# Kernel optimization log

Hardware: AMD Instinct MI355X
Metric: run time of the kernel (lower is better)

## Reference

```python
import jax, jax.numpy as jnp
import numpy as np
import math

N_NODES = 64000
N_GRAPHS = 512
HIDDEN = 128
CLUSTERS = 10
NUM_FILTER = 16
N_CLASSES = 2
S_HID = math.ceil((HIDDEN + CLUSTERS) / 2)  # 69
P_HID = 8


def _mlp2(x, w1, b1, w2, b2):
    # 2-layer MLP: Linear -> ReLU -> Linear (matches MLP(2, in, hid, out))
    return jax.nn.relu(x @ w1 + b1) @ w2 + b2


def setup_inputs() -> dict:
    key = jax.random.key(0)
    ks = jax.random.split(key, 12)
    # node embeddings (output of get_emb)
    H_all = jax.random.normal(ks[0], (N_NODES, HIDDEN), dtype=jnp.float32)
    # graph indicator: 125 nodes per graph, sorted (as produced by batching)
    batch = jnp.repeat(jnp.arange(N_GRAPHS, dtype=jnp.int32), N_NODES // N_GRAPHS)
    targets = jax.random.randint(ks[1], (N_GRAPHS,), 0, N_CLASSES, dtype=jnp.int32)
    s = 0.05
    # S_mlp: hidden -> S_HID -> clusters
    w1 = jax.random.normal(ks[2], (HIDDEN, S_HID), dtype=jnp.float32) * s
    b1 = jnp.zeros((S_HID,), dtype=jnp.float32)
    w2 = jax.random.normal(ks[3], (S_HID, CLUSTERS), dtype=jnp.float32) * s
    b2 = jnp.zeros((CLUSTERS,), dtype=jnp.float32)
    # final: hidden*clusters -> 2
    wf = jax.random.normal(ks[4], (HIDDEN * CLUSTERS, N_CLASSES), dtype=jnp.float32) * s
    bf = jnp.zeros((N_CLASSES,), dtype=jnp.float32)
    # prototype_features_MLP: hidden -> 8 -> num_graph_filter
    p1 = jax.random.normal(ks[5], (HIDDEN, P_HID), dtype=jnp.float32) * s
    pb1 = jnp.zeros((P_HID,), dtype=jnp.float32)
    p2 = jax.random.normal(ks[6], (P_HID, NUM_FILTER), dtype=jnp.float32) * s
    pb2 = jnp.zeros((NUM_FILTER,), dtype=jnp.float32)
    # correlation parameters (initialized like the torch module)
    corr_inter = jax.nn.softmax(jax.random.uniform(ks[7], (N_CLASSES, NUM_FILTER)), axis=0)
    corr_intra = jax.nn.softmax(jax.random.uniform(ks[8], (N_CLASSES, NUM_FILTER)), axis=1)
    return {"H_all": H_all, "batch": batch, "targets": targets,
            "w1": w1, "b1": b1, "w2": w2, "b2": b2,
            "wf": wf, "bf": bf,
            "p1": p1, "pb1": pb1, "p2": p2, "pb2": pb2,
            "corr_inter": corr_inter, "corr_intra": corr_intra}


def reference(H_all, batch, targets, w1, b1, w2, b2, wf, bf,
              p1, pb1, p2, pb2, corr_inter, corr_intra):
    # per-node soft cluster assignment  [N, C]
    S_all = jax.nn.softmax(_mlp2(H_all, w1, b1, w2, b2), axis=-1)
    # segment matmul E_g = S_g^T @ H_g  -> [B, C, D] via segment-reduced outer products
    outer = S_all[:, :, None] * H_all[:, None, :]  # [N, C, D]
    E_all = jax.ops.segment_sum(outer, batch, num_segments=N_GRAPHS)
    B = E_all.shape[0]
    pred1 = E_all.reshape(B, -1) @ wf + bf  # dropout off (eval)
    p = jax.nn.softmax(pred1, axis=-1)
    # multinomial sample from pred_softmax (no grad)
    key = jax.random.key(42)
    sample = jax.random.categorical(key, jnp.log(jax.lax.stop_gradient(p) + 1e-12), axis=-1)
    ind_positive_sample = sample == targets
    oh = jax.nn.one_hot(sample, N_CLASSES, dtype=p.dtype)
    epsilon = jax.lax.stop_gradient(jnp.where(oh != 0, 1.0 - p, -p))
    sample_cat_oh = p + epsilon  # straight-through one-hot
    Q = jax.nn.softmax(_mlp2(E_all, p1, pb1, p2, pb2), axis=-1)  # [B, C, F]
    correlation = jax.nn.softmax(corr_inter, axis=0) * jax.nn.softmax(corr_intra, axis=1)  # [2, F]
    correlation_mask = sample_cat_oh @ correlation  # [B, F]
    feature_mask = jnp.sum(Q * correlation_mask[:, None, :], axis=-1)  # [B, C]
    E_masked = feature_mask[:, :, None] * E_all  # einsum('bi,bij->bij')
    pred2 = E_masked.reshape(B, -1) @ wf + bf
    return (pred1, pred2, ind_positive_sample, S_all, E_all, Q)
```

## Files before the change

kernel.cpp:

```cpp
#include <hip/hip_runtime.h>

#define NN 64000
#define NG 512
#define NPG 125
#define DIM 128
#define NC 10
#define SHID 69
#define NF 16
#define PHID 8
#define ELPAD 132
#define TSTR 85
#define PSTR 41
#define EPSTR 11

#define OFF_PRED1 0
#define OFF_PRED2 1024
#define OFF_IND   2048
#define OFF_S     2560
#define OFF_E     642560
#define OFF_Q     1297920

typedef __attribute__((ext_vector_type(8))) short short8;
typedef __attribute__((ext_vector_type(4))) float f32x4;

__device__ __forceinline__ unsigned rotl32(unsigned x, int r) {
    return (x << r) | (x >> (32 - r));
}

__device__ __forceinline__ void threefry_0_42(unsigned x0, unsigned x1,
                                              unsigned& o0, unsigned& o1) {
    const unsigned k0 = 0u, k1 = 42u;
    const unsigned k2 = k0 ^ k1 ^ 0x1BD11BDAu;
    unsigned ks[3] = {k0, k1, k2};
    const int R0[4] = {13, 15, 26, 6};
    const int R1[4] = {17, 29, 16, 24};
    x0 += k0; x1 += k1;
    #pragma unroll
    for (int i = 0; i < 5; i++) {
        const int* R = (i & 1) ? R1 : R0;
        #pragma unroll
        for (int r = 0; r < 4; r++) {
            x0 += x1;
            x1 = rotl32(x1, R[r]);
            x1 ^= x0;
        }
        x0 += ks[(i + 1) % 3];
        x1 += ks[(i + 2) % 3] + (unsigned)(i + 1);
    }
    o0 = x0; o1 = x1;
}

__device__ __forceinline__ unsigned random_bits_partitionable(unsigned i) {
    unsigned o0, o1;
    threefry_0_42(0u, i, o0, o1);
    return o0 ^ o1;
}

__device__ __forceinline__ float gumbel_from_bits(unsigned bits) {
    float f = __uint_as_float((bits >> 9) | 0x3f800000u) - 1.0f;
    if (f <= 0.0f) f = 1.1754943508222875e-38f;
    return -logf(-logf(f));
}

#define R10(M) M(0) M(1) M(2) M(3) M(4) M(5) M(6) M(7) M(8) M(9)

__global__ __launch_bounds__(256) void k_split_w1(
    const float* __restrict__ w1, short* __restrict__ fragHi,
    short* __restrict__ fragLo) {
    int e = blockIdx.x * 256 + threadIdx.x;
    int s = e >> 3, i = e & 7;
    int jt = s >> 8, ks = (s >> 6) & 3, l = s & 63;
    int j = jt * 16 + (l & 15);
    int kb = ks * 32 + ((l >> 4) & 3) * 8;
    float x = (j < SHID) ? w1[(kb + i) * SHID + j] : 0.0f;
    unsigned u = __float_as_uint(x);
    short hi = (short)(u >> 16);
    float hf = __uint_as_float(u & 0xFFFF0000u);
    short lo = (short)(__float_as_uint(x - hf) >> 16);
    fragHi[s * 8 + i] = hi;
    fragLo[s * 8 + i] = lo;
}

__global__ __launch_bounds__(256, 4) void k_node_mlp(
    const float* __restrict__ H, const short* __restrict__ fragHi,
    const short* __restrict__ fragLo,
    const float* __restrict__ b1, const float* __restrict__ w2,
    const float* __restrict__ b2, float* __restrict__ S) {
    __shared__ __align__(16) float Ts[64 * TSTR];
    __shared__ float Ps[64 * PSTR];
    int tid = threadIdx.x;
    int w = tid >> 6, l = tid & 63;
    int node = blockIdx.x * 64 + w * 16 + (l & 15);
    const float* Hp = H + (size_t)node * DIM + ((l >> 4) & 3) * 8;

    short8 aHi[4], aLo[4];
    #pragma unroll
    for (int ks = 0; ks < 4; ks++) {
        float4 x0 = *(const float4*)(Hp + ks * 32);
        float4 x1 = *(const float4*)(Hp + ks * 32 + 4);
        float xs[8] = {x0.x, x0.y, x0.z, x0.w, x1.x, x1.y, x1.z, x1.w};
        #pragma unroll
        for (int i = 0; i < 8; i++) {
            unsigned u = __float_as_uint(xs[i]);
            aHi[ks][i] = (short)(u >> 16);
            float lo = xs[i] - __uint_as_float(u & 0xFFFF0000u);
            aLo[ks][i] = (short)(__float_as_uint(lo) >> 16);
        }
    }

    f32x4 acc[5];
    #pragma unroll
    for (int jt = 0; jt < 5; jt++) {
        f32x4 a = {0.f, 0.f, 0.f, 0.f};
        #pragma unroll
        for (int ks = 0; ks < 4; ks++) {
            int slot = (jt * 4 + ks) * 64 + l;
            short8 bh = *(const short8*)(fragHi + (size_t)slot * 8);
            short8 bl = *(const short8*)(fragLo + (size_t)slot * 8);
            a = __builtin_amdgcn_mfma_f32_16x16x32_bf16(aHi[ks], bh, a, 0, 0, 0);
            a = __builtin_amdgcn_mfma_f32_16x16x32_bf16(aLo[ks], bh, a, 0, 0, 0);
            a = __builtin_amdgcn_mfma_f32_16x16x32_bf16(aHi[ks], bl, a, 0, 0, 0);
        }
        acc[jt] = a;
    }

    #pragma unroll
    for (int jt = 0; jt < 5; jt++) {
        int j = jt * 16 + (l & 15);
        float bj = (j < SHID) ? b1[j] : 0.0f;
        #pragma unroll
        for (int r = 0; r < 4; r++) {
            int m = w * 16 + ((l >> 4) & 3) * 4 + r;
            float tv = acc[jt][r];
            Ts[m * TSTR + j] = (j < SHID) ? fmaxf(tv + bj, 0.0f) : 0.0f;
        }
    }
    __syncthreads();

    {
        int n = tid & 63, q = tid >> 6;
        float lg[NC] = {};
        for (int jj = 0; jj < 18; jj++) {
            int j = q * 18 + jj;
            int jx = (j < SHID) ? j : (SHID - 1);
            float tr = Ts[n * TSTR + j];
            const float* w2r = w2 + jx * NC;
            #pragma unroll
            for (int c = 0; c < NC; c++) lg[c] = fmaf(tr, w2r[c], lg[c]);
        }
        #pragma unroll
        for (int c = 0; c < NC; c++) Ps[n * PSTR + q * NC + c] = lg[c];
    }
    __syncthreads();

    if (tid < 64) {
        int n = tid;
        const float* pr = &Ps[n * PSTR];
        #define LD(c) float s##c = pr[c] + pr[10 + c] + pr[20 + c] + pr[30 + c] + b2[c];
        R10(LD)
        #undef LD
        float m = fmaxf(fmaxf(fmaxf(s0, s1), fmaxf(s2, s3)),
                        fmaxf(fmaxf(fmaxf(s4, s5), fmaxf(s6, s7)), fmaxf(s8, s9)));
        float e0 = expf(s0 - m), e1 = expf(s1 - m), e2 = expf(s2 - m),
              e3 = expf(s3 - m), e4 = expf(s4 - m), e5 = expf(s5 - m),
              e6 = expf(s6 - m), e7 = expf(s7 - m), e8 = expf(s8 - m),
              e9 = expf(s9 - m);
        float ssum = ((e0 + e1) + (e2 + e3)) + ((e4 + e5) + (e6 + e7)) + (e8 + e9);
        float inv = 1.0f / ssum;
        float2* Sp2 = (float2*)(S + ((size_t)blockIdx.x * 64 + n) * NC);
        Sp2[0] = make_float2(e0 * inv, e1 * inv);
        Sp2[1] = make_float2(e2 * inv, e3 * inv);
        Sp2[2] = make_float2(e4 * inv, e5 * inv);
        Sp2[3] = make_float2(e6 * inv, e7 * inv);
        Sp2[4] = make_float2(e8 * inv, e9 * inv);
    }
}

__global__ __launch_bounds__(1024, 4) void k_E_tail(
    const float* __restrict__ H, const float* __restrict__ S,
    const float* __restrict__ wf, const float* __restrict__ bf,
    const int* __restrict__ targets,
    const float* __restrict__ p1, const float* __restrict__ pb1,
    const float* __restrict__ p2, const float* __restrict__ pb2,
    const float* __restrict__ ci, const float* __restrict__ cr,
    float* __restrict__ E, float* __restrict__ pred1, float* __restrict__ pred2,
    float* __restrict__ ind, float* __restrict__ Q) {
    __shared__ __align__(8) float Sl[128 * NC];
    __shared__ float Epart[7 * 128 * EPSTR];
    __shared__ __align__(16) float El[NC * ELPAD];
    __shared__ float fmbuf[NC];
    int g = blockIdx.x, tid = threadIdx.x;

    const float* Sg = S + (size_t)g * NPG * NC;
    for (int i = tid; i < 128 * NC; i += 1024) Sl[i] = (i < NPG * NC) ? Sg[i] : 0.0f;
    __syncthreads();

    int q = tid >> 7;
    int d = tid & 127;
    const float* Hg = H + (size_t)g * NPG * DIM + d;

    #define DECLA(c) float a##c = 0.f;
    R10(DECLA)
    #undef DECLA
    int n0 = q * 16;
    #pragma unroll
    for (int ib = 0; ib < 16; ib += 8) {
        float h[8];
        #pragma unroll
        for (int u = 0; u < 8; u++) {
            int nh = min(n0 + ib + u, NPG - 1);
            h[u] = Hg[(size_t)nh * DIM];
        }
        #pragma unroll
        for (int u = 0; u < 8; u++) {
            const float2* S2 = (const float2*)(Sl + (n0 + ib + u) * NC);
            float2 s01 = S2[0], s23 = S2[1], s45 = S2[2], s67 = S2[3], s89 = S2[4];
            a0 = fmaf(s01.x, h[u], a0); a1 = fmaf(s01.y, h[u], a1);
            a2 = fmaf(s23.x, h[u], a2); a3 = fmaf(s23.y, h[u], a3);
            a4 = fmaf(s45.x, h[u], a4); a5 = fmaf(s45.y, h[u], a5);
            a6 = fmaf(s67.x, h[u], a6); a7 = fmaf(s67.y, h[u], a7);
            a8 = fmaf(s89.x, h[u], a8); a9 = fmaf(s89.y, h[u], a9);
        }
    }
    if (q > 0) {
        float* ep = &Epart[((q - 1) * 128 + d) * EPSTR];
        #define STP(c) ep[c] = a##c;
        R10(STP)
        #undef STP
    }
    __syncthreads();
    if (q == 0) {
        float* Eo = E + (size_t)g * (NC * DIM) + d;
        #pragma unroll
        for (int k = 0; k < 7; k++) {
            const float* ep = &Epart[(k * 128 + d) * EPSTR];
            a0 += ep[0]; a1 += ep[1]; a2 += ep[2]; a3 += ep[3]; a4 += ep[4];
            a5 += ep[5]; a6 += ep[6]; a7 += ep[7]; a8 += ep[8]; a9 += ep[9];
        }
        #define CMB(c) { El[(c) * ELPAD + d] = a##c; Eo[(c) * DIM] = a##c; }
        R10(CMB)
        #undef CMB
    }
    __syncthreads();

    const float2* wf2 = (const float2*)wf;
    int l = tid;
    int samp = 0;
    float corr_lf = 0.f;

    if (tid < 64) {
        if (l < 32) {
            int i = l >> 4, f = l & 15;
            float a = ci[f], b = ci[NF + f];
            float mm = fmaxf(a, b);
            float ea = expf(a - mm), eb = expf(b - mm);
            float inter = expf(ci[i * NF + f] - mm) / (ea + eb);
            float mi = -1e30f;
            for (int j = 0; j < NF; j++) mi = fmaxf(mi, cr[i * NF + j]);
            float ri = 0.f;
            for (int j = 0; j < NF; j++) ri += expf(cr[i * NF + j] - mi);
            float intra = expf(cr[i * NF + f] - mi) / ri;
            corr_lf = inter * intra;
        }

        float a0 = 0.f, a1 = 0.f;
        #pragma unroll
        for (int i = 0; i < 20; i++) {
            int idx = i * 64 + l;
            float e = El[(idx >> 7) * ELPAD + (idx & 127)];
            float2 w = wf2[idx];
            a0 = fmaf(e, w.x, a0);
            a1 = fmaf(e, w.y, a1);
        }
        #pragma unroll
        for (int off = 32; off > 0; off >>= 1) {
            a0 += __shfl_down(a0, off);
            a1 += __shfl_down(a1, off);
        }
        if (l == 0) {
            float y0 = a0 + bf[0], y1 = a1 + bf[1];
            pred1[g * 2] = y0;
            pred1[g * 2 + 1] = y1;
            float m = fmaxf(y0, y1);
            float e0 = expf(y0 - m), e1 = expf(y1 - m), s = e0 + e1;
            float p0 = e0 / s, pp1 = e1 / s;
            float g0 = gumbel_from_bits(random_bits_partitionable(2 * g));
            float g1 = gumbel_from_bits(random_bits_partitionable(2 * g + 1));
            float l0 = logf(p0 + 1e-12f) + g0;
            float l1 = logf(pp1 + 1e-12f) + g1;
            samp = (l1 > l0) ? 1 : 0;
            ind[g] = (samp == targets[g]) ? 1.0f : 0.0f;
        }
        samp = __shfl(samp, 0);

        if (l < 40) {
            int p = l >> 2, s = l & 3;
            float ua = pb1[2 * s], ub = pb1[2 * s + 1];
            const float4* E4 = (const float4*)&El[p * ELPAD];
            #pragma unroll 4
            for (int k4 = 0; k4 < 32; k4++) {
                float4 e4 = E4[k4];
                float es[4] = {e4.x, e4.y, e4.z, e4.w};
                #pragma unroll
                for (int kk = 0; kk < 4; kk++) {
                    int k = k4 * 4 + kk;
                    ua = fmaf(es[kk], p1[k * PHID + 2 * s], ua);
                    ub = fmaf(es[kk], p1[k * PHID + 2 * s + 1], ub);
                }
            }
            ua = fmaxf(ua, 0.f);
            ub = fmaxf(ub, 0.f);
            float v[NF];
            #pragma unroll
            for (int f = 0; f < NF; f++) {
                v[f] = pb2[f] * 0.25f;
                v[f] = fmaf(ua, p2[(2 * s) * NF + f], v[f]);
                v[f] = fmaf(ub, p2[(2 * s + 1) * NF + f], v[f]);
            }
            #pragma unroll
            for (int f = 0; f < NF; f++) {
                v[f] += __shfl_xor(v[f], 1);
                v[f] += __shfl_xor(v[f], 2);
            }
            float m = v[0];
            #pragma unroll
            for (int f = 1; f < NF; f++) m = fmaxf(m, v[f]);
            float ssum = 0.f, qv[NF];
            #pragma unroll
            for (int f = 0; f < NF; f++) { qv[f] = expf(v[f] - m); ssum += qv[f]; }
            float inv = 1.0f / ssum;
            #pragma unroll
            for (int f = 0; f < NF; f++) qv[f] *= inv;
            float* Qo = Q + ((size_t)g * NC + p) * NF;
            ((float4*)Qo)[s] = make_float4(qv[s * 4], qv[s * 4 + 1], qv[s * 4 + 2], qv[s * 4 + 3]);
            float fmv = 0.f;
            #pragma unroll
            for (int f = 0; f < NF; f++) {
                float cv = __shfl(corr_lf, samp * NF + f);
                fmv = fmaf(qv[f], cv, fmv);
            }
            if (s == 0) fmbuf[p] = fmv;
        }
    }
    __syncthreads();

    if (tid < 64) {
        float b0 = 0.f, b1acc = 0.f;
        #pragma unroll
        for (int i = 0; i < 20; i++) {
            int idx = i * 64 + l;
            float e = El[(idx >> 7) * ELPAD + (idx & 127)] * fmbuf[idx >> 7];
            float2 w = wf2[idx];
            b0 = fmaf(e, w.x, b0);
            b1acc = fmaf(e, w.y, b1acc);
        }
        #pragma unroll
        for (int off = 32; off > 0; off >>= 1) {
            b0 += __shfl_down(b0, off);
            b1acc += __shfl_down(b1acc, off);
        }
        if (l == 0) {
            pred2[g * 2] = b0 + bf[0];
            pred2[g * 2 + 1] = b1acc + bf[1];
        }
    }
}

extern "C" void kernel_launch(void* const* d_in, const int* in_sizes, int n_in,
                              void* d_out, int out_size, void* d_ws, size_t ws_size,
                              hipStream_t stream) {
    const float* H       = (const float*)d_in[0];
    const int*   targets = (const int*)d_in[2];
    const float* w1      = (const float*)d_in[3];
    const float* b1      = (const float*)d_in[4];
    const float* w2      = (const float*)d_in[5];
    const float* b2      = (const float*)d_in[6];
    const float* wf      = (const float*)d_in[7];
    const float* bf      = (const float*)d_in[8];
    const float* p1      = (const float*)d_in[9];
    const float* pb1     = (const float*)d_in[10];
    const float* p2      = (const float*)d_in[11];
    const float* pb2     = (const float*)d_in[12];
    const float* ci      = (const float*)d_in[13];
    const float* cr      = (const float*)d_in[14];

    float* out   = (float*)d_out;
    float* pred1 = out + OFF_PRED1;
    float* pred2 = out + OFF_PRED2;
    float* ind   = out + OFF_IND;
    float* S     = out + OFF_S;
    float* E     = out + OFF_E;
    float* Q     = out + OFF_Q;

    short* fragHi = (short*)d_ws;
    short* fragLo = (short*)((char*)d_ws + 20480);

    k_split_w1<<<40, 256, 0, stream>>>(w1, fragHi, fragLo);
    k_node_mlp<<<NN / 64, 256, 0, stream>>>(H, fragHi, fragLo, b1, w2, b2, S);
    k_E_tail<<<NG, 1024, 0, stream>>>(H, S, wf, bf, targets, p1, pb1, p2, pb2,
                                      ci, cr, E, pred1, pred2, ind, Q);
}
```

Measured before the change: 132.6 us.

## Fuse node MLP softmax into per-graph segment-sum kernel

Merges the per-node MLP/softmax kernel with the per-graph E/tail kernel, so each 512-thread block computes S for its graph's 125 nodes, keeps it in shared memory, then reduces the outer products. This removes a kernel launch and the global round trip of S, and H rows are read twice within the same block, likely hitting cache. The second layer of the MLP now runs in registers with cross-lane shuffles instead of shared-memory staging. Only 512 blocks of 512 threads are launched, which lowers parallelism for the MFMA phase and gives each thread more serial work.

```diff
diff --git a/kernel.cpp b/kernel.cpp
--- a/kernel.cpp
+++ b/kernel.cpp
@@ -9,8 +9,6 @@
 #define NF 16
 #define PHID 8
 #define ELPAD 132
-#define TSTR 85
-#define PSTR 41
 #define EPSTR 11
 
 #define OFF_PRED1 0
@@ -81,176 +79,188 @@
     fragLo[s * 8 + i] = lo;
 }
 
-__global__ __launch_bounds__(256, 4) void k_node_mlp(
+__global__ __launch_bounds__(512, 2) void k_fused(
     const float* __restrict__ H, const short* __restrict__ fragHi,
     const short* __restrict__ fragLo,
     const float* __restrict__ b1, const float* __restrict__ w2,
-    const float* __restrict__ b2, float* __restrict__ S) {
-    __shared__ __align__(16) float Ts[64 * TSTR];
-    __shared__ float Ps[64 * PSTR];
-    int tid = threadIdx.x;
-    int w = tid >> 6, l = tid & 63;
-    int node = blockIdx.x * 64 + w * 16 + (l & 15);
-    const float* Hp = H + (size_t)node * DIM + ((l >> 4) & 3) * 8;
-
-    short8 aHi[4], aLo[4];
-    #pragma unroll
-    for (int ks = 0; ks < 4; ks++) {
-        float4 x0 = *(const float4*)(Hp + ks * 32);
-        float4 x1 = *(const float4*)(Hp + ks * 32 + 4);
-        float xs[8] = {x0.x, x0.y, x0.z, x0.w, x1.x, x1.y, x1.z, x1.w};
-        #pragma unroll
-        for (int i = 0; i < 8; i++) {
-            unsigned u = __float_as_uint(xs[i]);
-            aHi[ks][i] = (short)(u >> 16);
-            float lo = xs[i] - __uint_as_float(u & 0xFFFF0000u);
-            aLo[ks][i] = (short)(__float_as_uint(lo) >> 16);
-        }
-    }
-
-    f32x4 acc[5];
-    #pragma unroll
-    for (int jt = 0; jt < 5; jt++) {
-        f32x4 a = {0.f, 0.f, 0.f, 0.f};
-        #pragma unroll
-        for (int ks = 0; ks < 4; ks++) {
-            int slot = (jt * 4 + ks) * 64 + l;
-            short8 bh = *(const short8*)(fragHi + (size_t)slot * 8);
-            short8 bl = *(const short8*)(fragLo + (size_t)slot * 8);
-            a = __builtin_amdgcn_mfma_f32_16x16x32_bf16(aHi[ks], bh, a, 0, 0, 0);
-            a = __builtin_amdgcn_mfma_f32_16x16x32_bf16(aLo[ks], bh, a, 0, 0, 0);
-            a = __builtin_amdgcn_mfma_f32_16x16x32_bf16(aHi[ks], bl, a, 0, 0, 0);
-        }
-        acc[jt] = a;
-    }
-
-    #pragma unroll
-    for (int jt = 0; jt < 5; jt++) {
-        int j = jt * 16 + (l & 15);
-        float bj = (j < SHID) ? b1[j] : 0.0f;
-        #pragma unroll
-        for (int r = 0; r < 4; r++) {
-            int m = w * 16 + ((l >> 4) & 3) * 4 + r;
-            float tv = acc[jt][r];
-            Ts[m * TSTR + j] = (j < SHID) ? fmaxf(tv + bj, 0.0f) : 0.0f;
-        }
-    }
-    __syncthreads();
-
-    {
-        int n = tid & 63, q = tid >> 6;
-        float lg[NC] = {};
-        for (int jj = 0; jj < 18; jj++) {
-            int j = q * 18 + jj;
-            int jx = (j < SHID) ? j : (SHID - 1);
-            float tr = Ts[n * TSTR + j];
-            const float* w2r = w2 + jx * NC;
-            #pragma unroll
-            for (int c = 0; c < NC; c++) lg[c] = fmaf(tr, w2r[c], lg[c]);
-        }
-        #pragma unroll
-        for (int c = 0; c < NC; c++) Ps[n * PSTR + q * NC + c] = lg[c];
-    }
-    __syncthreads();
-
-    if (tid < 64) {
-        int n = tid;
-        const float* pr = &Ps[n * PSTR];
-        #define LD(c) float s##c = pr[c] + pr[10 + c] + pr[20 + c] + pr[30 + c] + b2[c];
-        R10(LD)
-        #undef LD
-        float m = fmaxf(fmaxf(fmaxf(s0, s1), fmaxf(s2, s3)),
-                        fmaxf(fmaxf(fmaxf(s4, s5), fmaxf(s6, s7)), fmaxf(s8, s9)));
-        float e0 = expf(s0 - m), e1 = expf(s1 - m), e2 = expf(s2 - m),
-              e3 = expf(s3 - m), e4 = expf(s4 - m), e5 = expf(s5 - m),
-              e6 = expf(s6 - m), e7 = expf(s7 - m), e8 = expf(s8 - m),
-              e9 = expf(s9 - m);
-        float ssum = ((e0 + e1) + (e2 + e3)) + ((e4 + e5) + (e6 + e7)) + (e8 + e9);
-        float inv = 1.0f / ssum;
-        float2* Sp2 = (float2*)(S + ((size_t)blockIdx.x * 64 + n) * NC);
-        Sp2[0] = make_float2(e0 * inv, e1 * inv);
-        Sp2[1] = make_float2(e2 * inv, e3 * inv);
-        Sp2[2] = make_float2(e4 * inv, e5 * inv);
-        Sp2[3] = make_float2(e6 * inv, e7 * inv);
-        Sp2[4] = make_float2(e8 * inv, e9 * inv);
-    }
-}
-
-__global__ __launch_bounds__(1024, 4) void k_E_tail(
-    const float* __restrict__ H, const float* __restrict__ S,
+    const float* __restrict__ b2,
     const float* __restrict__ wf, const float* __restrict__ bf,
     const int* __restrict__ targets,
     const float* __restrict__ p1, const float* __restrict__ pb1,
     const float* __restrict__ p2, const float* __restrict__ pb2,
     const float* __restrict__ ci, const float* __restrict__ cr,
-    float* __restrict__ E, float* __restrict__ pred1, float* __restrict__ pred2,
+    float* __restrict__ S, float* __restrict__ E,
+    float* __restrict__ pred1, float* __restrict__ pred2,
     float* __restrict__ ind, float* __restrict__ Q) {
     __shared__ __align__(8) float Sl[128 * NC];
-    __shared__ float Epart[7 * 128 * EPSTR];
+    __shared__ float Epart[3 * 128 * EPSTR];
     __shared__ __align__(16) float El[NC * ELPAD];
     __shared__ float fmbuf[NC];
     int g = blockIdx.x, tid = threadIdx.x;
-
-    const float* Sg = S + (size_t)g * NPG * NC;
-    for (int i = tid; i < 128 * NC; i += 1024) Sl[i] = (i < NPG * NC) ? Sg[i] : 0.0f;
-    __syncthreads();
-
-    int q = tid >> 7;
-    int d = tid & 127;
-    const float* Hg = H + (size_t)g * NPG * DIM + d;
-
-    #define DECLA(c) float a##c = 0.f;
-    R10(DECLA)
-    #undef DECLA
-    int n0 = q * 16;
-    #pragma unroll
-    for (int ib = 0; ib < 16; ib += 8) {
-        float h[8];
-        #pragma unroll
-        for (int u = 0; u < 8; u++) {
-            int nh = min(n0 + ib + u, NPG - 1);
-            h[u] = Hg[(size_t)nh * DIM];
-        }
-        #pragma unroll
-        for (int u = 0; u < 8; u++) {
-            const float2* S2 = (const float2*)(Sl + (n0 + ib + u) * NC);
-            float2 s01 = S2[0], s23 = S2[1], s45 = S2[2], s67 = S2[3], s89 = S2[4];
-            a0 = fmaf(s01.x, h[u], a0); a1 = fmaf(s01.y, h[u], a1);
-            a2 = fmaf(s23.x, h[u], a2); a3 = fmaf(s23.y, h[u], a3);
-            a4 = fmaf(s45.x, h[u], a4); a5 = fmaf(s45.y, h[u], a5);
-            a6 = fmaf(s67.x, h[u], a6); a7 = fmaf(s67.y, h[u], a7);
-            a8 = fmaf(s89.x, h[u], a8); a9 = fmaf(s89.y, h[u], a9);
-        }
-    }
-    if (q > 0) {
-        float* ep = &Epart[((q - 1) * 128 + d) * EPSTR];
-        #define STP(c) ep[c] = a##c;
-        R10(STP)
-        #undef STP
+    int w = tid >> 6, l = tid & 63;
+    int lm = l & 15, quad = (l >> 4) & 3;
+
+    {
+        int nload = w * 16 + lm;
+        int nclamp = min(nload, NPG - 1);
+        const float* Hp = H + ((size_t)g * NPG + nclamp) * DIM + quad * 8;
+
+        short8 aHi[4], aLo[4];
+        #pragma unroll
+        for (int ks = 0; ks < 4; ks++) {
+            float4 x0 = *(const float4*)(Hp + ks * 32);
+            float4 x1 = *(const float4*)(Hp + ks * 32 + 4);
+            float xs[8] = {x0.x, x0.y, x0.z, x0.w, x1.x, x1.y, x1.z, x1.w};
+            #pragma unroll
+            for (int i = 0; i < 8; i++) {
+                unsigned u = __float_as_uint(xs[i]);
+                aHi[ks][i] = (short)(u >> 16);
+                float lo = xs[i] - __uint_as_float(u & 0xFFFF0000u);
+                aLo[ks][i] = (short)(__float_as_uint(lo) >> 16);
+            }
+        }
+
+        f32x4 acc[5];
+        #pragma unroll
+        for (int jt = 0; jt < 5; jt++) {
+            f32x4 a = {0.f, 0.f, 0.f, 0.f};
+            #pragma unroll
+            for (int ks = 0; ks < 4; ks++) {
+                int slot = (jt * 4 + ks) * 64 + l;
+                short8 bh = *(const short8*)(fragHi + (size_t)slot * 8);
+                short8 bl = *(const short8*)(fragLo + (size_t)slot * 8);
+                a = __builtin_amdgcn_mfma_f32_16x16x32_bf16(aHi[ks], bh, a, 0, 0, 0);
+                a = __builtin_amdgcn_mfma_f32_16x16x32_bf16(aLo[ks], bh, a, 0, 0, 0);
+                a = __builtin_amdgcn_mfma_f32_16x16x32_bf16(aHi[ks], bl, a, 0, 0, 0);
+            }
+            acc[jt] = a;
+        }
+
+        float lg[4][10] = {};
+        #pragma unroll
+        for (int jt = 0; jt < 5; jt++) {
+            int j = jt * 16 + lm;
+            bool jv = (j < SHID);
+            int jx = jv ? j : 0;
+            float bj = b1[jx];
+            float wv[10];
+            const float* w2r = w2 + jx * NC;
+            #pragma unroll
+            for (int c = 0; c < NC; c++) wv[c] = w2r[c];
+            #pragma unroll
+            for (int r = 0; r < 4; r++) {
+                float tr = jv ? fmaxf(acc[jt][r] + bj, 0.0f) : 0.0f;
+                #pragma unroll
+                for (int c = 0; c < NC; c++) lg[r][c] = fmaf(tr, wv[c], lg[r][c]);
+            }
+        }
+        #pragma unroll
+        for (int r = 0; r < 4; r++) {
+            #pragma unroll
+            for (int c = 0; c < NC; c++) {
+                lg[r][c] += __shfl_xor(lg[r][c], 1);
+                lg[r][c] += __shfl_xor(lg[r][c], 2);
+                lg[r][c] += __shfl_xor(lg[r][c], 4);
+                lg[r][c] += __shfl_xor(lg[r][c], 8);
+            }
+        }
+
+        if (lm == 0) {
+            #pragma unroll
+            for (int r = 0; r < 4; r++) {
+                int nloc = w * 16 + quad * 4 + r;
+                bool valid = (nloc < NPG);
+                float s0 = lg[r][0] + b2[0], s1 = lg[r][1] + b2[1],
+                      s2 = lg[r][2] + b2[2], s3 = lg[r][3] + b2[3],
+                      s4 = lg[r][4] + b2[4], s5 = lg[r][5] + b2[5],
+                      s6 = lg[r][6] + b2[6], s7 = lg[r][7] + b2[7],
+                      s8 = lg[r][8] + b2[8], s9 = lg[r][9] + b2[9];
+                float m = fmaxf(fmaxf(fmaxf(s0, s1), fmaxf(s2, s3)),
+                                fmaxf(fmaxf(fmaxf(s4, s5), fmaxf(s6, s7)),
+                                      fmaxf(s8, s9)));
+                float e0 = expf(s0 - m), e1 = expf(s1 - m), e2 = expf(s2 - m),
+                      e3 = expf(s3 - m), e4 = expf(s4 - m), e5 = expf(s5 - m),
+                      e6 = expf(s6 - m), e7 = expf(s7 - m), e8 = expf(s8 - m),
+                      e9 = expf(s9 - m);
+                float ssum = ((e0 + e1) + (e2 + e3)) + ((e4 + e5) + (e6 + e7)) + (e8 + e9);
+                float inv = valid ? (1.0f / ssum) : 0.0f;
+                float v0 = e0 * inv, v1 = e1 * inv, v2 = e2 * inv, v3 = e3 * inv,
+                      v4 = e4 * inv, v5 = e5 * inv, v6 = e6 * inv, v7 = e7 * inv,
+                      v8 = e8 * inv, v9 = e9 * inv;
+                float* slp = &Sl[nloc * NC];
+                slp[0] = v0; slp[1] = v1; slp[2] = v2; slp[3] = v3; slp[4] = v4;
+                slp[5] = v5; slp[6] = v6; slp[7] = v7; slp[8] = v8; slp[9] = v9;
+                if (valid) {
+                    float2* Sp2 = (float2*)(S + ((size_t)g * NPG + nloc) * NC);
+                    Sp2[0] = make_float2(v0, v1);
+                    Sp2[1] = make_float2(v2, v3);
+                    Sp2[2] = make_float2(v4, v5);
+                    Sp2[3] = make_float2(v6, v7);
+                    Sp2[4] = make_float2(v8, v9);
+                }
+            }
+        }
     }
     __syncthreads();
-    if (q == 0) {
-        float* Eo = E + (size_t)g * (NC * DIM) + d;
-        #pragma unroll
-        for (int k = 0; k < 7; k++) {
-            const float* ep = &Epart[(k * 128 + d) * EPSTR];
-            a0 += ep[0]; a1 += ep[1]; a2 += ep[2]; a3 += ep[3]; a4 += ep[4];
-            a5 += ep[5]; a6 += ep[6]; a7 += ep[7]; a8 += ep[8]; a9 += ep[9];
-        }
-        #define CMB(c) { El[(c) * ELPAD + d] = a##c; Eo[(c) * DIM] = a##c; }
-        R10(CMB)
-        #undef CMB
+
+    {
+        int q = tid >> 7;
+        int d = tid & 127;
+        const float* Hg = H + (size_t)g * NPG * DIM + d;
+
+        #define DECLA(c) float a##c = 0.f;
+        R10(DECLA)
+        #undef DECLA
+        int n0 = q * 32;
+        #pragma unroll
+        for (int ib = 0; ib < 32; ib += 8) {
+            float h[8];
+            #pragma unroll
+            for (int u = 0; u < 8; u++) {
+                int nh = min(n0 + ib + u, NPG - 1);
+                h[u] = Hg[(size_t)nh * DIM];
+            }
+            #pragma unroll
+            for (int u = 0; u < 8; u++) {
+                const float2* S2 = (const float2*)(Sl + (n0 + ib + u) * NC);
+                float2 s01 = S2[0], s23 = S2[1], s45 = S2[2], s67 = S2[3], s89 = S2[4];
+                a0 = fmaf(s01.x, h[u], a0); a1 = fmaf(s01.y, h[u], a1);
+                a2 = fmaf(s23.x, h[u], a2); a3 = fmaf(s23.y, h[u], a3);
+                a4 = fmaf(s45.x, h[u], a4); a5 = fmaf(s45.y, h[u], a5);
+                a6 = fmaf(s67.x, h[u], a6); a7 = fmaf(s67.y, h[u], a7);
+                a8 = fmaf(s89.x, h[u], a8); a9 = fmaf(s89.y, h[u], a9);
+            }
+        }
+        if (q > 0) {
+            float* ep = &Epart[((q - 1) * 128 + d) * EPSTR];
+            #define STP(c) ep[c] = a##c;
+            R10(STP)
+            #undef STP
+        }
+        __syncthreads();
+        if (q == 0) {
+            float* Eo = E + (size_t)g * (NC * DIM) + d;
+            #pragma unroll
+            for (int k = 0; k < 3; k++) {
+                const float* ep = &Epart[(k * 128 + d) * EPSTR];
+                a0 += ep[0]; a1 += ep[1]; a2 += ep[2]; a3 += ep[3]; a4 += ep[4];
+                a5 += ep[5]; a6 += ep[6]; a7 += ep[7]; a8 += ep[8]; a9 += ep[9];
+            }
+            #define CMB(c) { El[(c) * ELPAD + d] = a##c; Eo[(c) * DIM] = a##c; }
+            R10(CMB)
+            #undef CMB
+        }
     }
     __syncthreads();
 
     const float2* wf2 = (const float2*)wf;
-    int l = tid;
+    int lt = tid;
     int samp = 0;
     float corr_lf = 0.f;
 
     if (tid < 64) {
-        if (l < 32) {
-            int i = l >> 4, f = l & 15;
+        if (lt < 32) {
+            int i = lt >> 4, f = lt & 15;
             float a = ci[f], b = ci[NF + f];
             float mm = fmaxf(a, b);
             float ea = expf(a - mm), eb = expf(b - mm);
@@ -266,18 +276,18 @@
         float a0 = 0.f, a1 = 0.f;
         #pragma unroll
         for (int i = 0; i < 20; i++) {
-            int idx = i * 64 + l;
+            int idx = i * 64 + lt;
             float e = El[(idx >> 7) * ELPAD + (idx & 127)];
-            float2 w = wf2[idx];
-            a0 = fmaf(e, w.x, a0);
-            a1 = fmaf(e, w.y, a1);
+            float2 wv = wf2[idx];
+            a0 = fmaf(e, wv.x, a0);
+            a1 = fmaf(e, wv.y, a1);
         }
         #pragma unroll
         for (int off = 32; off > 0; off >>= 1) {
             a0 += __shfl_down(a0, off);
             a1 += __shfl_down(a1, off);
         }
-        if (l == 0) {
+        if (lt == 0) {
             float y0 = a0 + bf[0], y1 = a1 + bf[1];
             pred1[g * 2] = y0;
             pred1[g * 2 + 1] = y1;
@@ -293,8 +303,8 @@
         }
         samp = __shfl(samp, 0);
 
-        if (l < 40) {
-            int p = l >> 2, s = l & 3;
+        if (lt < 40) {
+            int p = lt >> 2, s = lt & 3;
             float ua = pb1[2 * s], ub = pb1[2 * s + 1];
             const float4* E4 = (const float4*)&El[p * ELPAD];
             #pragma unroll 4
@@ -348,18 +358,18 @@
         float b0 = 0.f, b1acc = 0.f;
         #pragma unroll
         for (int i = 0; i < 20; i++) {
-            int idx = i * 64 + l;
+            int idx = i * 64 + lt;
             float e = El[(idx >> 7) * ELPAD + (idx & 127)] * fmbuf[idx >> 7];
-            float2 w = wf2[idx];
-            b0 = fmaf(e, w.x, b0);
-            b1acc = fmaf(e, w.y, b1acc);
+            float2 wv = wf2[idx];
+            b0 = fmaf(e, wv.x, b0);
+            b1acc = fmaf(e, wv.y, b1acc);
         }
         #pragma unroll
         for (int off = 32; off > 0; off >>= 1) {
             b0 += __shfl_down(b0, off);
             b1acc += __shfl_down(b1acc, off);
         }
-        if (l == 0) {
+        if (lt == 0) {
             pred2[g * 2] = b0 + bf[0];
             pred2[g * 2 + 1] = b1acc + bf[1];
         }
@@ -396,7 +406,7 @@
     short* fragLo = (short*)((char*)d_ws + 20480);
 
     k_split_w1<<<40, 256, 0, stream>>>(w1, fragHi, fragLo);
-    k_node_mlp<<<NN / 64, 256, 0, stream>>>(H, fragHi, fragLo, b1, w2, b2, S);
-    k_E_tail<<<NG, 1024, 0, stream>>>(H, S, wf, bf, targets, p1, pb1, p2, pb2,
-                                      ci, cr, E, pred1, pred2, ind, Q);
-}
+    k_fused<<<NG, 512, 0, stream>>>(H, fragHi, fragLo, b1, w2, b2, wf, bf,
+                                    targets, p1, pb1, p2, pb2, ci, cr,
+                                    S, E, pred1, pred2, ind, Q);
+}
```

Measured after the change: 132.0 us. Within noise of the previous version (-0.4%).
